# Kernel tuning notes

Measured on AMD Instinct MI355X. Metric: run time of the kernel, lower is better.

The kernel has to match this reference:

```python
import jax, jax.numpy as jnp
import numpy as np


def setup_inputs() -> dict:
    key = jax.random.key(0)
    k1, k2, k3 = jax.random.split(key, 3)
    B, C, H, W = 16, 32, 48, 48
    inp = jax.random.normal(k1, (B, C, H, W), dtype=jnp.float32)
    # weight channels encode a CxC matrix per pixel; add identity (in the
    # flattened C*C channel layout) so every per-pixel matrix is well
    # conditioned for solve/slogdet, as a trained flow's weights would be.
    w = jax.random.normal(k2, (B, C * C, H, W), dtype=jnp.float32) * 0.1
    eye = jnp.eye(C, dtype=jnp.float32).reshape(C * C, 1, 1)
    w = w + eye
    logdet = jax.random.normal(k3, (B,), dtype=jnp.float32)
    return {"input": inp, "weight": w, "logdet": logdet}


def reference(input, weight, logdet):
    # forward (reverse=False) path of InvConditionalLinear
    B, C, H, W = input.shape
    # [B, C*C, H, W] -> [B, H, W, C, C] per-pixel matrices
    w = jnp.transpose(weight, (0, 2, 3, 1)).reshape(B, H, W, C, C)
    # sum of per-pixel log|det W| over all pixels -> [B]
    weight_logdet = jnp.sum(jnp.linalg.slogdet(w)[1], axis=(1, 2))
    # batched per-pixel solve: W z = x
    rhs = jnp.transpose(input, (0, 2, 3, 1))[..., None]  # [B,H,W,C,1]
    z = jnp.linalg.solve(w, rhs)[..., 0]                  # [B,H,W,C]
    z = jnp.transpose(z, (0, 3, 1, 2))                    # [B,C,H,W]
    return z, logdet - weight_logdet
```

## Files before the change

kernel.cpp:

```cpp
#include <hip/hip_runtime.h>
#include <math.h>

#define CDIM 32
#define HWDIM 2304
#define BDIM 16
#define PPW 8
#define NTHREADS 256
#define PPB 32
#define ZOFF (BDIM * CDIM * HWDIM)

__global__ __launch_bounds__(NTHREADS, 2)
void solve_kernel(const float* __restrict__ input,
                  const float* __restrict__ weight,
                  const float* __restrict__ logdet,
                  float* __restrict__ out) {
    const int t    = threadIdx.x;
    const int lane = t & 63;
    const int wv   = t >> 6;
    const int h    = lane & 7;
    const int p    = lane >> 3;
    const int gb   = lane & 56;

    const int blk  = blockIdx.x;
    const int b    = blk / (HWDIM / PPB);
    const int pix0 = (blk % (HWDIM / PPB)) * PPB + wv * PPW;
    const int pix  = pix0 + p;

    const float* wp = weight + (size_t)b * (CDIM * CDIM) * HWDIM
                             + (size_t)(h * CDIM) * HWDIM + pix;
    const float* xp = input + (size_t)b * CDIM * HWDIM + (size_t)h * HWDIM + pix;

    float A[4][CDIM];
    float y[4];
    #pragma unroll
    for (int r = 0; r < 4; ++r) {
        #pragma unroll
        for (int j = 0; j < CDIM; ++j)
            A[r][j] = wp[(size_t)(r * 8 * CDIM + j) * HWDIM];
        y[r] = xp[(size_t)(r * 8) * HWDIM];
    }

    float lacc = 0.0f;
    #pragma unroll
    for (int k = 0; k < CDIM; ++k) {
        const int tr = k >> 3, k7 = k & 7;
        const int src = gb + k7;
        float bp = __shfl(A[tr][k], src);
        float r  = __builtin_amdgcn_rcpf(bp);
        lacc += __log2f(fabsf(bp));

        float m[4];
        m[tr] = (h > k7) ? A[tr][k] * r : ((h == k7) ? (1.0f - r) : 0.0f);
        #pragma unroll
        for (int q = tr + 1; q < 4; ++q) m[q] = A[q][k] * r;

        #pragma unroll
        for (int j = k + 1; j < CDIM; ++j) {
            float bv = __shfl(A[tr][j], src);
            #pragma unroll
            for (int q = tr; q < 4; ++q)
                A[q][j] = fmaf(-m[q], bv, A[q][j]);
        }
        float bq = __shfl(y[tr], src);
        #pragma unroll
        for (int q = tr; q < 4; ++q) y[q] = fmaf(-m[q], bq, y[q]);
    }

    #pragma unroll
    for (int k = CDIM - 1; k >= 1; --k) {
        const int tr = k >> 3, k7 = k & 7;
        const int src = gb + k7;
        float bz = __shfl(y[tr], src);
        float c = (h < k7) ? A[tr][k] : 0.0f;
        y[tr] = fmaf(-c, bz, y[tr]);
        #pragma unroll
        for (int q = 0; q < tr; ++q)
            y[q] = fmaf(-A[q][k], bz, y[q]);
    }

    float* zp = out + (size_t)b * CDIM * HWDIM + (size_t)h * HWDIM + pix;
    #pragma unroll
    for (int r = 0; r < 4; ++r) zp[(size_t)(r * 8) * HWDIM] = y[r];

    float v = lacc;
    v += __shfl_xor(v, 8);
    v += __shfl_xor(v, 16);
    v += __shfl_xor(v, 32);
    if (lane == 0) {
        float add = -v * 0.69314718055994531f;
        if (pix0 == 0) add += logdet[b];
        atomicAdd(&out[ZOFF + b], add);
    }
}

extern "C" void kernel_launch(void* const* d_in, const int* in_sizes, int n_in,
                              void* d_out, int out_size, void* d_ws, size_t ws_size,
                              hipStream_t stream) {
    const float* input  = (const float*)d_in[0];
    const float* weight = (const float*)d_in[1];
    const float* logdet = (const float*)d_in[2];
    float* out = (float*)d_out;

    solve_kernel<<<BDIM * (HWDIM / PPB), NTHREADS, 0, stream>>>(input, weight,
                                                                logdet, out);
}
```

Baseline: 266.3 us.

## Split each pixel's matrix across 16 lanes instead of 8 to cut registers

Each per-pixel 32x32 Gauss-Jordan solve is now spread over 16 lanes, each holding 2 rows, instead of 8 lanes holding 4 rows. This roughly halves the register footprint per thread, and launch bounds now target 4 blocks per SIMD for higher occupancy and better latency hiding on the strided weight loads. The cost is twice as many threads doing the same shuffles per pixel, so the total shuffle count and redundant broadcast work per pixel goes up.

```diff
diff --git a/kernel.cpp b/kernel.cpp
--- a/kernel.cpp
+++ b/kernel.cpp
@@ -4,12 +4,12 @@
 #define CDIM 32
 #define HWDIM 2304
 #define BDIM 16
-#define PPW 8
+#define PPW 4
 #define NTHREADS 256
-#define PPB 32
+#define PPB 16
 #define ZOFF (BDIM * CDIM * HWDIM)
 
-__global__ __launch_bounds__(NTHREADS, 2)
+__global__ __launch_bounds__(NTHREADS, 4)
 void solve_kernel(const float* __restrict__ input,
                   const float* __restrict__ weight,
                   const float* __restrict__ logdet,
@@ -17,78 +17,78 @@
     const int t    = threadIdx.x;
     const int lane = t & 63;
     const int wv   = t >> 6;
-    const int h    = lane & 7;
-    const int p    = lane >> 3;
-    const int gb   = lane & 56;
+    const int h    = lane & 15;
+    const int p    = lane >> 4;
+    const int gb   = lane & 48;
 
     const int blk  = blockIdx.x;
     const int b    = blk / (HWDIM / PPB);
-    const int pix0 = (blk % (HWDIM / PPB)) * PPB + wv * PPW;
-    const int pix  = pix0 + p;
+    const int pg   = blk % (HWDIM / PPB);
+    const int pix  = pg * PPB + wv * PPW + p;
 
     const float* wp = weight + (size_t)b * (CDIM * CDIM) * HWDIM
                              + (size_t)(h * CDIM) * HWDIM + pix;
     const float* xp = input + (size_t)b * CDIM * HWDIM + (size_t)h * HWDIM + pix;
 
-    float A[4][CDIM];
-    float y[4];
+    float ylo = xp[0];
+    float yhi = xp[(size_t)(16 * HWDIM)];
+
+    float Alo[CDIM], Ahi[CDIM];
     #pragma unroll
-    for (int r = 0; r < 4; ++r) {
-        #pragma unroll
-        for (int j = 0; j < CDIM; ++j)
-            A[r][j] = wp[(size_t)(r * 8 * CDIM + j) * HWDIM];
-        y[r] = xp[(size_t)(r * 8) * HWDIM];
+    for (int j = 0; j < CDIM; ++j) {
+        Alo[j] = wp[(size_t)j * HWDIM];
+        Ahi[j] = wp[(size_t)(16 * CDIM + j) * HWDIM];
     }
 
     float lacc = 0.0f;
     #pragma unroll
     for (int k = 0; k < CDIM; ++k) {
-        const int tr = k >> 3, k7 = k & 7;
-        const int src = gb + k7;
-        float bp = __shfl(A[tr][k], src);
+        const int src = gb + (k & 15);
+        float bp = __shfl((k < 16) ? Alo[k] : Ahi[k], src);
         float r  = __builtin_amdgcn_rcpf(bp);
         lacc += __log2f(fabsf(bp));
 
-        float m[4];
-        m[tr] = (h > k7) ? A[tr][k] * r : ((h == k7) ? (1.0f - r) : 0.0f);
-        #pragma unroll
-        for (int q = tr + 1; q < 4; ++q) m[q] = A[q][k] * r;
-
+        float mlo = 0.0f, mhi;
+        if (k < 16) {
+            mlo = (h == k) ? (1.0f - r) : ((h > k) ? Alo[k] * r : 0.0f);
+            mhi = Ahi[k] * r;
+        } else {
+            mhi = (h + 16 == k) ? (1.0f - r)
+                                : ((h + 16 > k) ? Ahi[k] * r : 0.0f);
+        }
         #pragma unroll
         for (int j = k + 1; j < CDIM; ++j) {
-            float bv = __shfl(A[tr][j], src);
-            #pragma unroll
-            for (int q = tr; q < 4; ++q)
-                A[q][j] = fmaf(-m[q], bv, A[q][j]);
+            float bv = __shfl((k < 16) ? Alo[j] : Ahi[j], src);
+            if (k < 16) Alo[j] = fmaf(-mlo, bv, Alo[j]);
+            Ahi[j] = fmaf(-mhi, bv, Ahi[j]);
         }
-        float bq = __shfl(y[tr], src);
-        #pragma unroll
-        for (int q = tr; q < 4; ++q) y[q] = fmaf(-m[q], bq, y[q]);
+        float bq = __shfl((k < 16) ? ylo : yhi, src);
+        if (k < 16) ylo = fmaf(-mlo, bq, ylo);
+        yhi = fmaf(-mhi, bq, yhi);
     }
 
     #pragma unroll
     for (int k = CDIM - 1; k >= 1; --k) {
-        const int tr = k >> 3, k7 = k & 7;
-        const int src = gb + k7;
-        float bz = __shfl(y[tr], src);
-        float c = (h < k7) ? A[tr][k] : 0.0f;
-        y[tr] = fmaf(-c, bz, y[tr]);
-        #pragma unroll
-        for (int q = 0; q < tr; ++q)
-            y[q] = fmaf(-A[q][k], bz, y[q]);
+        const int src = gb + (k & 15);
+        float bz = __shfl((k < 16) ? ylo : yhi, src);
+        if (k >= 17) {
+            float chi = (h + 16 < k) ? Ahi[k] : 0.0f;
+            yhi = fmaf(-chi, bz, yhi);
+        }
+        float clo = (k >= 16) ? Alo[k] : ((h < k) ? Alo[k] : 0.0f);
+        ylo = fmaf(-clo, bz, ylo);
     }
 
     float* zp = out + (size_t)b * CDIM * HWDIM + (size_t)h * HWDIM + pix;
-    #pragma unroll
-    for (int r = 0; r < 4; ++r) zp[(size_t)(r * 8) * HWDIM] = y[r];
+    zp[0] = ylo;
+    zp[(size_t)(16 * HWDIM)] = yhi;
 
     float v = lacc;
-    v += __shfl_xor(v, 8);
     v += __shfl_xor(v, 16);
     v += __shfl_xor(v, 32);
     if (lane == 0) {
         float add = -v * 0.69314718055994531f;
-        if (pix0 == 0) add += logdet[b];
+        if (pg == 0 && wv == 0) add += logdet[b];
         atomicAdd(&out[ZOFF + b], add);
     }
 }
```

After: 871.6 us. 227% more time.
